# Optimization experiments

Measured on AMD Instinct MI355X. Metric: run time of the kernel, lower is better.

## Reference

```python
import jax, jax.numpy as jnp
import numpy as np

N = 20000      # nodes
E = 320000     # edges (avg in-degree 16)
R = 100        # relation types
F = 256        # in_ent_feats == out_ent_feats == in_rel_feats
H = 8          # heads
D = F // H     # head dim = 32
HOP = 5        # PPR hops
ALPHA = 0.1
SLOPE = 0.2    # LeakyReLU negative slope


def _ln(x, g, b, eps=1e-5):
    m = x.mean(-1, keepdims=True)
    v = ((x - m) ** 2).mean(-1, keepdims=True)
    return (x - m) / jnp.sqrt(v + eps) * g + b


def setup_inputs() -> dict:
    key = jax.random.key(0)
    ks = jax.random.split(key, 12)
    s = 1.0 / np.sqrt(F)
    ent_feat = jax.random.normal(ks[0], (N, F), jnp.float32)
    rel_feat = jax.random.normal(ks[1], (R, F), jnp.float32)
    W_head = jax.random.normal(ks[2], (F, F), jnp.float32) * s
    W_tail = jax.random.normal(ks[3], (F, F), jnp.float32) * s
    W_ent = jax.random.normal(ks[4], (F, F), jnp.float32) * s
    W_rel = jax.random.normal(ks[5], (F, F), jnp.float32) * s
    attn = jax.random.normal(ks[6], (1, H, D), jnp.float32) * s
    ln_ent_g = jnp.ones((F,), jnp.float32); ln_ent_b = jnp.zeros((F,), jnp.float32)
    ln_rel_g = jnp.ones((F,), jnp.float32); ln_rel_b = jnp.zeros((F,), jnp.float32)
    ln_ff_g = jnp.ones((F,), jnp.float32); ln_ff_b = jnp.zeros((F,), jnp.float32)
    W1 = jax.random.normal(ks[7], (F, 4 * F), jnp.float32) * s
    b1 = jnp.zeros((4 * F,), jnp.float32)
    W2 = jax.random.normal(ks[8], (4 * F, F), jnp.float32) * (0.5 * s)
    b2 = jnp.zeros((F,), jnp.float32)
    src = jax.random.randint(ks[9], (E,), 0, N, dtype=jnp.int32)
    # every node must have in-degree >= 1 (DGL raises on 0-in-degree nodes)
    dst = jnp.concatenate([jnp.arange(N, dtype=jnp.int32),
                           jax.random.randint(ks[10], (E - N,), 0, N, dtype=jnp.int32)])
    rid = jax.random.randint(ks[11], (E,), 0, R, dtype=jnp.int32)
    return {"ent_feat": ent_feat, "rel_feat": rel_feat,
            "W_head": W_head, "W_tail": W_tail, "W_ent": W_ent, "W_rel": W_rel,
            "attn": attn,
            "ln_ent_g": ln_ent_g, "ln_ent_b": ln_ent_b,
            "ln_rel_g": ln_rel_g, "ln_rel_b": ln_rel_b,
            "ln_ff_g": ln_ff_g, "ln_ff_b": ln_ff_b,
            "W1": W1, "b1": b1, "W2": W2, "b2": b2,
            "src": src, "dst": dst, "rid": rid}


def reference(ent_feat, rel_feat, W_head, W_tail, W_ent, W_rel, attn,
              ln_ent_g, ln_ent_b, ln_rel_g, ln_rel_b, ln_ff_g, ln_ff_b,
              W1, b1, W2, b2, src, dst, rid):
    n = ent_feat.shape[0]
    x = _ln(ent_feat, ln_ent_g, ln_ent_b)                 # [N,F]
    fh = (x @ W_head).reshape(n, H, D)                    # 'eh'
    ftl = (x @ W_tail).reshape(n, H, D)                   # 'et'
    fen = (x @ W_ent).reshape(n, H, D)                    # 'ft'
    r = _ln(rel_feat, ln_rel_g, ln_rel_b)
    fr = (r @ W_rel).reshape(-1, H, D)[rid]               # [E,H,D]
    # relational edge attention score
    e = jax.nn.leaky_relu(fh[src] * ftl[dst] * fr, SLOPE)
    e = (e * attn).sum(-1)                                # [E,H]
    # e_mul_v with log in-degree, scaled by head_dim
    deg = jax.ops.segment_sum(jnp.ones((src.shape[0],), e.dtype), dst, num_segments=n)
    e = e * (jnp.log(deg)[dst])[:, None] / D
    # edge softmax over incoming edges of each dst node, per head
    m = jax.lax.stop_gradient(jax.ops.segment_max(e, dst, num_segments=n))
    ex = jnp.exp(e - m[dst])
    denom = jax.ops.segment_sum(ex, dst, num_segments=n)
    a = ex / denom[dst]                                   # [E,H]
    # PPR-style diffusion aggregation
    feat0 = fen
    feat = fen
    for _ in range(HOP):
        msg = feat[src] * a[:, :, None]                   # [E,H,D]
        agg = jax.ops.segment_sum(msg, dst, num_segments=n)
        feat = (1.0 - ALPHA) * agg + ALPHA * feat0
    # residual (Identity since in_ent_feats == out_ent_feats)
    rst = feat + ent_feat.reshape(n, H, D)
    rst = rst.reshape(n, F)
    # position-wise feed-forward with pre-LN and residual
    y = _ln(rst, ln_ff_g, ln_ff_b)
    ff = jax.nn.relu(y @ W1 + b1) @ W2 + b2
    return ff + rst
```

## Files before the change

kernel.cpp:

```cpp
#include <hip/hip_runtime.h>

#define N_NODES 20000
#define N_EDGES 320000
#define N_REL   100
#define FDIM    256
#define NHEAD   8
#define HDIM    32
#define SCAN_BLOCKS ((N_NODES + 255) / 256)

using short8 = __attribute__((ext_vector_type(8))) short;
using f32x4  = __attribute__((ext_vector_type(4))) float;

__device__ inline unsigned short f2bf(float f) {
    union { float f; unsigned int u; } v; v.f = f;
    unsigned int r = v.u + 0x7fff + ((v.u >> 16) & 1);
    return (unsigned short)(r >> 16);
}
__device__ inline float bf2f(unsigned short u) {
    union { unsigned int i; float f; } v; v.i = ((unsigned int)u) << 16; return v.f;
}
__device__ inline float4 bf4(ushort4 u) {
    return make_float4(bf2f(u.x), bf2f(u.y), bf2f(u.z), bf2f(u.w));
}
__device__ inline void unpack8(float* d, uint4 u) {
    union { unsigned int u; float f; } t;
    t.u = u.x << 16;         d[0] = t.f;
    t.u = u.x & 0xffff0000u; d[1] = t.f;
    t.u = u.y << 16;         d[2] = t.f;
    t.u = u.y & 0xffff0000u; d[3] = t.f;
    t.u = u.z << 16;         d[4] = t.f;
    t.u = u.z & 0xffff0000u; d[5] = t.f;
    t.u = u.w << 16;         d[6] = t.f;
    t.u = u.w & 0xffff0000u; d[7] = t.f;
}
__device__ inline void fma8(float* acc, uint4 u, float w) {
    union { unsigned int u; float f; } t;
    t.u = u.x << 16;         acc[0] += w * t.f;
    t.u = u.x & 0xffff0000u; acc[1] += w * t.f;
    t.u = u.y << 16;         acc[2] += w * t.f;
    t.u = u.y & 0xffff0000u; acc[3] += w * t.f;
    t.u = u.z << 16;         acc[4] += w * t.f;
    t.u = u.z & 0xffff0000u; acc[5] += w * t.f;
    t.u = u.w << 16;         acc[6] += w * t.f;
    t.u = u.w & 0xffff0000u; acc[7] += w * t.f;
}
__device__ __forceinline__ void g2lds16(const unsigned short* g, unsigned short* l) {
    __builtin_amdgcn_global_load_lds(
        (const __attribute__((address_space(1))) unsigned int*)g,
        (__attribute__((address_space(3))) unsigned int*)l,
        16, 0, 0);
}

__device__ inline void xcd_tile(int* m0, int* n0, int tm, int tn) {
    int nwg  = gridDim.x * gridDim.y;
    int wgid = blockIdx.x + blockIdx.y * gridDim.x;
    int q = nwg >> 3, r = nwg & 7;
    int xcd = wgid & 7, pos = wgid >> 3;
    int nid = (xcd < r ? xcd * (q + 1) : r * (q + 1) + (xcd - r) * q) + pos;
    int gy = gridDim.y;
    int bx = nid / gy;
    int by = nid - bx * gy;
    *m0 = bx * tm;
    *n0 = by * tn;
}

__global__ __launch_bounds__(64) void ln_fused_kernel(
    const float* __restrict__ ent, const float* __restrict__ rel,
    const float* __restrict__ ge, const float* __restrict__ be,
    const float* __restrict__ gr, const float* __restrict__ br,
    unsigned short* __restrict__ xb, unsigned short* __restrict__ rlnb)
{
    int row = blockIdx.x;
    const float *in, *g, *b; unsigned short* out; int r;
    if (row < N_NODES) { in = ent; g = ge; b = be; out = xb;   r = row; }
    else               { in = rel; g = gr; b = br; out = rlnb; r = row - N_NODES; }
    int tid = threadIdx.x;
    const float4 v = *(const float4*)(in + (size_t)r * FDIM + tid * 4);
    float s = v.x + v.y + v.z + v.w;
    float q = v.x * v.x + v.y * v.y + v.z * v.z + v.w * v.w;
    #pragma unroll
    for (int d = 1; d < 64; d <<= 1) { s += __shfl_xor(s, d); q += __shfl_xor(q, d); }
    float mean = s * (1.0f / FDIM);
    float var  = q * (1.0f / FDIM) - mean * mean;
    float inv  = rsqrtf(var + 1e-5f);
    float4 gg = *(const float4*)(g + tid * 4);
    float4 bb = *(const float4*)(b + tid * 4);
    ushort4 o;
    o.x = f2bf((v.x - mean) * inv * gg.x + bb.x);
    o.y = f2bf((v.y - mean) * inv * gg.y + bb.y);
    o.z = f2bf((v.z - mean) * inv * gg.z + bb.z);
    o.w = f2bf((v.w - mean) * inv * gg.w + bb.w);
    *(ushort4*)(out + (size_t)r * FDIM + tid * 4) = o;
}

__global__ __launch_bounds__(64) void rst_ln_kernel(
    const unsigned short* __restrict__ feat, const float* __restrict__ ent,
    const float* __restrict__ g, const float* __restrict__ b,
    float* __restrict__ rst, unsigned short* __restrict__ y)
{
    int row = blockIdx.x;
    int tid = threadIdx.x;
    const float4 f = bf4(*(const ushort4*)(feat + (size_t)row * FDIM + tid * 4));
    const float4 e = *(const float4*)(ent + (size_t)row * FDIM + tid * 4);
    float4 r;
    r.x = f.x + e.x; r.y = f.y + e.y; r.z = f.z + e.z; r.w = f.w + e.w;
    *(float4*)(rst + (size_t)row * FDIM + tid * 4) = r;
    float s = r.x + r.y + r.z + r.w;
    float q = r.x * r.x + r.y * r.y + r.z * r.z + r.w * r.w;
    #pragma unroll
    for (int d = 1; d < 64; d <<= 1) { s += __shfl_xor(s, d); q += __shfl_xor(q, d); }
    float mean = s * (1.0f / FDIM);
    float var  = q * (1.0f / FDIM) - mean * mean;
    float inv  = rsqrtf(var + 1e-5f);
    float4 gg = *(const float4*)(g + tid * 4);
    float4 bb = *(const float4*)(b + tid * 4);
    ushort4 o;
    o.x = f2bf((r.x - mean) * inv * gg.x + bb.x);
    o.y = f2bf((r.y - mean) * inv * gg.y + bb.y);
    o.z = f2bf((r.z - mean) * inv * gg.z + bb.z);
    o.w = f2bf((r.w - mean) * inv * gg.w + bb.w);
    *(ushort4*)(y + (size_t)row * FDIM + tid * 4) = o;
}

__global__ void transpose_all_kernel(
    const float* __restrict__ Wh, const float* __restrict__ Wt_,
    const float* __restrict__ We, const float* __restrict__ Wr,
    const float* __restrict__ W1, const float* __restrict__ W2,
    unsigned short* __restrict__ WtP, unsigned short* __restrict__ WtR,
    unsigned short* __restrict__ W1t, unsigned short* __restrict__ W2t)
{
    int idx = blockIdx.x * 256 + threadIdx.x;
    if (idx < 196608) {
        int seg = idx >> 16, r = idx & 65535;
        const float* W = (seg == 0) ? Wh : (seg == 1) ? Wt_ : We;
        int n = r >> 8, k = r & 255;
        WtP[idx] = f2bf(W[k * 256 + n]);
    } else if (idx < 262144) {
        int r = idx - 196608;
        int n = r >> 8, k = r & 255;
        WtR[r] = f2bf(Wr[k * 256 + n]);
    } else if (idx < 524288) {
        int r = idx - 262144;
        int n = r >> 8, k = r & 255;
        W1t[r] = f2bf(W1[k * 1024 + n]);
    } else if (idx < 786432) {
        int r = idx - 524288;
        int n = r >> 10, k = r & 1023;
        W2t[r] = f2bf(W2[k * 256 + n]);
    }
}

__global__ __launch_bounds__(256) void mfma_gemm_bt(
    const unsigned short* __restrict__ A, const unsigned short* __restrict__ Bt,
    const float* __restrict__ bias, const float* __restrict__ add,
    float* __restrict__ Cf, unsigned short* __restrict__ Cb,
    int M, int K, int N, int relu)
{
    __shared__ unsigned short As[2][128 * 32];
    __shared__ unsigned short Bs[2][128 * 32];
    int tid  = threadIdx.x;
    int wave = tid >> 6, lane = tid & 63;
    int quad = lane >> 4, l16 = lane & 15;
    int m0, n0;
    xcd_tile(&m0, &n0, 128, 128);
    int wr = (wave >> 1) * 64, wc = (wave & 1) * 64;

    f32x4 acc[4][4] = {};

    int cA = tid, cB = tid + 256;
    int rA0 = cA >> 2, kA0 = (cA & 3) * 8;
    int rB0 = cB >> 2, kB0 = (cB & 3) * 8;
    int rA = m0 + rA0; if (rA >= M) rA = M - 1;
    int rB = m0 + rB0; if (rB >= M) rB = M - 1;
    const unsigned short* gA0 = A + (size_t)rA * K + kA0;
    const unsigned short* gA1 = A + (size_t)rB * K + kB0;
    const unsigned short* gB0 = Bt + (size_t)(n0 + rA0) * K + kA0;
    const unsigned short* gB1 = Bt + (size_t)(n0 + rB0) * K + kB0;

    g2lds16(gA0, As[0] + cA * 8);
    g2lds16(gA1, As[0] + cB * 8);
    g2lds16(gB0, Bs[0] + cA * 8);
    g2lds16(gB1, Bs[0] + cB * 8);
    __syncthreads();

    int cur = 0;
    for (int k0 = 0; k0 < K; k0 += 32) {
        int k1 = k0 + 32;
        if (k1 < K) {
            int nb = cur ^ 1;
            g2lds16(gA0 + k1, As[nb] + cA * 8);
            g2lds16(gA1 + k1, As[nb] + cB * 8);
            g2lds16(gB0 + k1, Bs[nb] + cA * 8);
            g2lds16(gB1 + k1, Bs[nb] + cB * 8);
        }
        short8 af[4], bfr[4];
        #pragma unroll
        for (int i = 0; i < 4; ++i)
            af[i] = *(const short8*)(As[cur] + (wr + i * 16 + l16) * 32 + quad * 8);
        #pragma unroll
        for (int j = 0; j < 4; ++j)
            bfr[j] = *(const short8*)(Bs[cur] + (wc + j * 16 + l16) * 32 + quad * 8);
        #pragma unroll
        for (int i = 0; i < 4; ++i)
            #pragma unroll
            for (int j = 0; j < 4; ++j)
                acc[i][j] = __builtin_amdgcn_mfma_f32_16x16x32_bf16(
                    af[i], bfr[j], acc[i][j], 0, 0, 0);
        __syncthreads();
        cur ^= 1;
    }

    #pragma unroll
    for (int i = 0; i < 4; ++i) {
        #pragma unroll
        for (int j = 0; j < 4; ++j) {
            int col = n0 + wc + j * 16 + l16;
            float bsv = bias ? bias[col] : 0.0f;
            #pragma unroll
            for (int r = 0; r < 4; ++r) {
                int row = m0 + wr + i * 16 + quad * 4 + r;
                if (row < M) {
                    float v = acc[i][j][r] + bsv;
                    if (relu) v = fmaxf(v, 0.0f);
                    if (add)  v += add[(size_t)row * N + col];
                    if (Cf) Cf[(size_t)row * N + col] = v;
                    else    Cb[(size_t)row * N + col] = f2bf(v);
                }
            }
        }
    }
}

__global__ __launch_bounds__(256) void mfma_gemm64_bt(
    const unsigned short* __restrict__ A, const unsigned short* __restrict__ Bt,
    const float* __restrict__ bias, const float* __restrict__ add,
    float* __restrict__ Cf, int M, int K, int N)
{
    __shared__ unsigned short As[2][64 * 32];
    __shared__ unsigned short Bs[2][128 * 32];
    int tid  = threadIdx.x;
    int wave = tid >> 6, lane = tid & 63;
    int quad = lane >> 4, l16 = lane & 15;
    int m0, n0;
    xcd_tile(&m0, &n0, 64, 128);
    int wc = wave * 32;

    f32x4 acc[4][2] = {};

    int rA0 = tid >> 2, kA0 = (tid & 3) * 8;
    int cB0 = tid, cB1 = tid + 256;
    int rB0 = cB0 >> 2, kB0 = (cB0 & 3) * 8;
    int rB1 = cB1 >> 2, kB1 = (cB1 & 3) * 8;
    int rA = m0 + rA0; if (rA >= M) rA = M - 1;
    const unsigned short* gA  = A + (size_t)rA * K + kA0;
    const unsigned short* gB0 = Bt + (size_t)(n0 + rB0) * K + kB0;
    const unsigned short* gB1 = Bt + (size_t)(n0 + rB1) * K + kB1;

    g2lds16(gA,  As[0] + tid * 8);
    g2lds16(gB0, Bs[0] + cB0 * 8);
    g2lds16(gB1, Bs[0] + cB1 * 8);
    __syncthreads();

    int cur = 0;
    for (int k0 = 0; k0 < K; k0 += 32) {
        int k1 = k0 + 32;
        if (k1 < K) {
            int nb = cur ^ 1;
            g2lds16(gA + k1,  As[nb] + tid * 8);
            g2lds16(gB0 + k1, Bs[nb] + cB0 * 8);
            g2lds16(gB1 + k1, Bs[nb] + cB1 * 8);
        }
        short8 af[4], bfr[2];
        #pragma unroll
        for (int i = 0; i < 4; ++i)
            af[i] = *(const short8*)(As[cur] + (i * 16 + l16) * 32 + quad * 8);
        #pragma unroll
        for (int j = 0; j < 2; ++j)
            bfr[j] = *(const short8*)(Bs[cur] + (wc + j * 16 + l16) * 32 + quad * 8);
        #pragma unroll
        for (int i = 0; i < 4; ++i)
            #pragma unroll
            for (int j = 0; j < 2; ++j)
                acc[i][j] = __builtin_amdgcn_mfma_f32_16x16x32_bf16(
                    af[i], bfr[j], acc[i][j], 0, 0, 0);
        __syncthreads();
        cur ^= 1;
    }

    #pragma unroll
    for (int i = 0; i < 4; ++i) {
        #pragma unroll
        for (int j = 0; j < 2; ++j) {
            int col = n0 + wc + j * 16 + l16;
            float bsv = bias ? bias[col] : 0.0f;
            #pragma unroll
            for (int r = 0; r < 4; ++r) {
                int row = m0 + i * 16 + quad * 4 + r;
                if (row < M) {
                    float v = acc[i][j][r] + bsv;
                    if (add) v += add[(size_t)row * N + col];
                    Cf[(size_t)row * N + col] = v;
                }
            }
        }
    }
}

__global__ void count_kernel(const int* __restrict__ dst, int* __restrict__ deg, int E)
{
    int i = blockIdx.x * blockDim.x + threadIdx.x;
    if (i < E) atomicAdd(&deg[dst[i]], 1);
}

__global__ __launch_bounds__(256) void scan1_kernel(
    const int* __restrict__ deg, int* __restrict__ offsets, int* __restrict__ bsum, int n)
{
    __shared__ int tmp[256];
    int tid = threadIdx.x;
    int i = blockIdx.x * 256 + tid;
    int v = (i < n) ? deg[i] : 0;
    tmp[tid] = v;
    __syncthreads();
    for (int d = 1; d < 256; d <<= 1) {
        int u = (tid >= d) ? tmp[tid - d] : 0;
        __syncthreads();
        tmp[tid] += u;
        __syncthreads();
    }
    if (i < n) offsets[i] = tmp[tid] - v;
    if (tid == 255) bsum[blockIdx.x] = tmp[255];
}

__global__ __launch_bounds__(128) void scan2_kernel(int* __restrict__ bsum, int nb)
{
    __shared__ int tmp[128];
    int tid = threadIdx.x;
    int v = (tid < nb) ? bsum[tid] : 0;
    tmp[tid] = v;
    __syncthreads();
    for (int d = 1; d < 128; d <<= 1) {
        int u = (tid >= d) ? tmp[tid - d] : 0;
        __syncthreads();
        tmp[tid] += u;
        __syncthreads();
    }
    if (tid < nb) bsum[tid] = tmp[tid] - v;
}

__global__ __launch_bounds__(256) void scan3_kernel(
    const int* __restrict__ deg, int* __restrict__ offsets,
    const int* __restrict__ bsum, int* __restrict__ cursor,
    float* __restrict__ logdeg, int n, int E)
{
    int i = blockIdx.x * 256 + threadIdx.x;
    if (i < n) {
        int o = offsets[i] + bsum[blockIdx.x];
        offsets[i] = o;
        cursor[i]  = o;
        logdeg[i]  = logf((float)deg[i]);
    }
    if (i == 0) offsets[n] = E;
}

__global__ void scatter_kernel(const int* __restrict__ dst, const int* __restrict__ src,
                               const int* __restrict__ rid, int* __restrict__ cursor,
                               int* __restrict__ csr_src, int* __restrict__ csr_rid, int E)
{
    int i = blockIdx.x * blockDim.x + threadIdx.x;
    if (i < E) {
        int p = atomicAdd(&cursor[dst[i]], 1);
        csr_src[p] = src[i];
        csr_rid[p] = rid[i];
    }
}

__global__ __launch_bounds__(256) void edge_score_csr_kernel(
    const unsigned short* __restrict__ proj,
    const unsigned short* __restrict__ frel,
    const float* __restrict__ attn,
    const int* __restrict__ csr_src, const int* __restrict__ csr_rid,
    const int* __restrict__ offsets, const float* __restrict__ logdeg,
    float* __restrict__ csr_a, float* __restrict__ invd, int n)
{
    int node = blockIdx.x * 4 + (threadIdx.x >> 6);
    if (node >= n) return;
    int tid = threadIdx.x & 63;
    int g = tid >> 4, li = tid & 15;
    int start = offsets[node], end = offsets[node + 1];
    float scale = logdeg[node] * (1.0f / 32.0f);

    float tv[16], at[16];
    {
        const unsigned short* tp = proj + (size_t)node * 768 + 256 + li * 16;
        uint4 a0 = *(const uint4*)tp, a1 = *(const uint4*)(tp + 8);
        unpack8(tv, a0); unpack8(tv + 8, a1);
        const float4* ap = (const float4*)(attn + li * 16);
        float4 f;
        f = ap[0]; at[0] = f.x; at[1] = f.y; at[2]  = f.z; at[3]  = f.w;
        f = ap[1]; at[4] = f.x; at[5] = f.y; at[6]  = f.z; at[7]  = f.w;
        f = ap[2]; at[8] = f.x; at[9] = f.y; at[10] = f.z; at[11] = f.w;
        f = ap[3]; at[12] = f.x; at[13] = f.y; at[14] = f.z; at[15] = f.w;
    }

    float denom = 0.f;
    for (int p = start; p < end; p += 8) {
        int  pe[2]; bool va[2]; uint4 h0[2], h1[2], r0[2], r1[2];
        #pragma unroll
        for (int t = 0; t < 2; ++t) {
            pe[t] = p + t * 4 + g;
            va[t] = pe[t] < end;
            int q = va[t] ? pe[t] : end - 1;
            int s = csr_src[q], r = csr_rid[q];
            const unsigned short* hp = proj + (size_t)s * 768 + li * 16;
            const unsigned short* rp = frel + (size_t)r * FDIM + li * 16;
            h0[t] = *(const uint4*)hp; h1[t] = *(const uint4*)(hp + 8);
            r0[t] = *(const uint4*)rp; r1[t] = *(const uint4*)(rp + 8);
        }
        #pragma unroll
        for (int t = 0; t < 2; ++t) {
            float hv[16], rv[16];
            unpack8(hv, h0[t]); unpack8(hv + 8, h1[t]);
            unpack8(rv, r0[t]); unpack8(rv + 8, r1[t]);
            float sum = 0.f;
            #pragma unroll
            for (int k = 0; k < 16; ++k) {
                float m = hv[k] * tv[k] * rv[k];
                m = (m > 0.f) ? m : 0.2f * m;
                sum += m * at[k];
            }
            sum += __shfl_xor(sum, 1);
            float ex = __expf(sum * scale);
            if (va[t] && ((li & 1) == 0)) {
                csr_a[(size_t)pe[t] * NHEAD + (li >> 1)] = ex;
                denom += ex;
            }
        }
    }
    denom += __shfl_xor(denom, 16);
    denom += __shfl_xor(denom, 32);
    if (g == 0 && (li & 1) == 0)
        invd[node * NHEAD + (li >> 1)] = 1.0f / denom;
}

__global__ __launch_bounds__(256) void diffuse_kernel(
    const unsigned short* __restrict__ fin, int fin_stride,
    const unsigned short* __restrict__ feat0,
    const float* __restrict__ a, const float* __restrict__ invd,
    const int* __restrict__ csr_src,
    const int* __restrict__ offsets, unsigned short* __restrict__ fout, int n)
{
    int node = blockIdx.x * 4 + (threadIdx.x >> 6);
    if (node >= n) return;
    int tid = threadIdx.x & 63;
    int g = tid >> 4, li = tid & 15;
    int hh = li >> 1;
    int start = offsets[node], end = offsets[node + 1];
    float wnorm = invd[node * NHEAD + hh];
    float acc[16] = {};

    for (int p = start; p < end; p += 16) {
        uint4 u0[4], u1[4]; float w[4];
        #pragma unroll
        for (int t = 0; t < 4; ++t) {
            int pe = p + t * 4 + g;
            int q = (pe < end) ? pe : end - 1;
            int s = csr_src[q];
            w[t] = (pe < end) ? a[(size_t)q * NHEAD + hh] : 0.0f;
            const unsigned short* rp = fin + (size_t)s * fin_stride + li * 16;
            u0[t] = *(const uint4*)(rp);
            u1[t] = *(const uint4*)(rp + 8);
        }
        #pragma unroll
        for (int t = 0; t < 4; ++t) {
            fma8(acc + 0, u0[t], w[t]);
            fma8(acc + 8, u1[t], w[t]);
        }
    }
    #pragma unroll
    for (int k = 0; k < 16; ++k) {
        acc[k] += __shfl_xor(acc[k], 16);
        acc[k] += __shfl_xor(acc[k], 32);
    }
    if (g == 0) {
        const unsigned short* f0p = feat0 + (size_t)node * 768 + li * 16;
        uint4 f0a = *(const uint4*)(f0p);
        uint4 f0b = *(const uint4*)(f0p + 8);
        float f0[16];
        unpack8(f0, f0a); unpack8(f0 + 8, f0b);
        unsigned short o[16];
        #pragma unroll
        for (int k = 0; k < 16; ++k)
            o[k] = f2bf(0.9f * acc[k] * wnorm + 0.1f * f0[k]);
        uint4* dst4 = (uint4*)(fout + (size_t)node * FDIM + li * 16);
        dst4[0] = *(uint4*)(o);
        dst4[1] = *(uint4*)(o + 8);
    }
}

extern "C" void kernel_launch(void* const* d_in, const int* in_sizes, int n_in,
                              void* d_out, int out_size, void* d_ws, size_t ws_size,
                              hipStream_t stream)
{
    const float* ent_feat = (const float*)d_in[0];
    const float* rel_feat = (const float*)d_in[1];
    const float* W_head   = (const float*)d_in[2];
    const float* W_tail   = (const float*)d_in[3];
    const float* W_ent    = (const float*)d_in[4];
    const float* W_rel    = (const float*)d_in[5];
    const float* attn     = (const float*)d_in[6];
    const float* ln_ent_g = (const float*)d_in[7];
    const float* ln_ent_b = (const float*)d_in[8];
    const float* ln_rel_g = (const float*)d_in[9];
    const float* ln_rel_b = (const float*)d_in[10];
    const float* ln_ff_g  = (const float*)d_in[11];
    const float* ln_ff_b  = (const float*)d_in[12];
    const float* W1       = (const float*)d_in[13];
    const float* b1       = (const float*)d_in[14];
    const float* W2       = (const float*)d_in[15];
    const float* b2       = (const float*)d_in[16];
    const int*   src      = (const int*)d_in[17];
    const int*   dst      = (const int*)d_in[18];
    const int*   rid      = (const int*)d_in[19];
    float* out = (float*)d_out;

    char* base = (char*)d_ws;
    auto carve = [&](size_t bytes) { char* p = base; base += (bytes + 255) & ~(size_t)255; return p; };
    unsigned short* xb    = (unsigned short*)carve((size_t)N_NODES * FDIM * 2);
    unsigned short* projb = (unsigned short*)carve((size_t)N_NODES * 768 * 2);
    unsigned short* rlnb  = (unsigned short*)carve((size_t)N_REL * FDIM * 2);
    unsigned short* frelb = (unsigned short*)carve((size_t)N_REL * FDIM * 2);
    unsigned short* WtP   = (unsigned short*)carve((size_t)768 * FDIM * 2);
    unsigned short* WtR   = (unsigned short*)carve((size_t)FDIM * FDIM * 2);
    unsigned short* W1t   = (unsigned short*)carve((size_t)1024 * FDIM * 2);
    unsigned short* W2t   = (unsigned short*)carve((size_t)FDIM * 1024 * 2);
    unsigned short* hb0   = (unsigned short*)carve((size_t)N_NODES * FDIM * 2);
    unsigned short* hb1   = (unsigned short*)carve((size_t)N_NODES * FDIM * 2);
    unsigned short* yb    = (unsigned short*)carve((size_t)N_NODES * FDIM * 2);
    unsigned short* t1b   = (unsigned short*)carve((size_t)N_NODES * 1024 * 2);
    float* rst     = (float*)carve((size_t)N_NODES * FDIM * 4);
    float* csr_a   = (float*)carve(((size_t)N_EDGES * NHEAD + 256) * 4);
    float* invd    = (float*)carve((size_t)N_NODES * NHEAD * 4);
    int*   csr_src = (int*)carve((size_t)(N_EDGES + 64) * 4);
    int*   csr_rid = (int*)carve((size_t)(N_EDGES + 64) * 4);
    int*   deg     = (int*)carve((size_t)N_NODES * 4);
    float* logdeg  = (float*)carve((size_t)N_NODES * 4);
    int*   offsets = (int*)carve((size_t)(N_NODES + 1) * 4);
    int*   cursor  = (int*)carve((size_t)N_NODES * 4);
    int*   bsum    = (int*)carve((size_t)SCAN_BLOCKS * 4);

    hipMemsetAsync(deg, 0, (size_t)N_NODES * 4, stream);

    ln_fused_kernel<<<N_NODES + N_REL, 64, 0, stream>>>(
        ent_feat, rel_feat, ln_ent_g, ln_ent_b, ln_rel_g, ln_rel_b, xb, rlnb);

    transpose_all_kernel<<<786432 / 256, 256, 0, stream>>>(
        W_head, W_tail, W_ent, W_rel, W1, W2, WtP, WtR, W1t, W2t);

    dim3 gproj((N_NODES + 127) / 128, 768 / 128);
    mfma_gemm_bt<<<gproj, 256, 0, stream>>>(xb, WtP, nullptr, nullptr, nullptr, projb,
                                            N_NODES, FDIM, 768, 0);
    dim3 grel(1, FDIM / 128);
    mfma_gemm_bt<<<grel, 256, 0, stream>>>(rlnb, WtR, nullptr, nullptr, nullptr, frelb,
                                           N_REL, FDIM, FDIM, 0);

    count_kernel<<<(N_EDGES + 255) / 256, 256, 0, stream>>>(dst, deg, N_EDGES);
    scan1_kernel<<<SCAN_BLOCKS, 256, 0, stream>>>(deg, offsets, bsum, N_NODES);
    scan2_kernel<<<1, 128, 0, stream>>>(bsum, SCAN_BLOCKS);
    scan3_kernel<<<SCAN_BLOCKS, 256, 0, stream>>>(deg, offsets, bsum, cursor, logdeg,
                                                  N_NODES, N_EDGES);
    scatter_kernel<<<(N_EDGES + 255) / 256, 256, 0, stream>>>(dst, src, rid, cursor,
                                                              csr_src, csr_rid, N_EDGES);

    edge_score_csr_kernel<<<(N_NODES + 3) / 4, 256, 0, stream>>>(
        projb, frelb, attn, csr_src, csr_rid, offsets, logdeg, csr_a, invd, N_NODES);

    const unsigned short* fen = projb + 512;
    int gdif = (N_NODES + 3) / 4;
    diffuse_kernel<<<gdif, 256, 0, stream>>>(fen, 768, fen, csr_a, invd, csr_src, offsets, hb0, N_NODES);
    diffuse_kernel<<<gdif, 256, 0, stream>>>(hb0, FDIM, fen, csr_a, invd, csr_src, offsets, hb1, N_NODES);
    diffuse_kernel<<<gdif, 256, 0, stream>>>(hb1, FDIM, fen, csr_a, invd, csr_src, offsets, hb0, N_NODES);
    diffuse_kernel<<<gdif, 256, 0, stream>>>(hb0, FDIM, fen, csr_a, invd, csr_src, offsets, hb1, N_NODES);
    diffuse_kernel<<<gdif, 256, 0, stream>>>(hb1, FDIM, fen, csr_a, invd, csr_src, offsets, hb0, N_NODES);

    rst_ln_kernel<<<N_NODES, 64, 0, stream>>>(hb0, ent_feat, ln_ff_g, ln_ff_b, rst, yb);

    dim3 gff1((N_NODES + 127) / 128, 1024 / 128);
    mfma_gemm_bt<<<gff1, 256, 0, stream>>>(yb, W1t, b1, nullptr, nullptr, t1b,
                                           N_NODES, FDIM, 1024, 1);
    dim3 gff2((N_NODES + 63) / 64, FDIM / 128);
    mfma_gemm64_bt<<<gff2, 256, 0, stream>>>(t1b, W2t, b2, rst, out,
                                             N_NODES, 1024, FDIM);
}
```

Measured before the change: 469.7 us.

## Load full K=256 tiles into swizzled LDS for GEMMs, hoist LDS reads in 64-row GEMM

```diff
diff --git a/kernel.cpp b/kernel.cpp
--- a/kernel.cpp
+++ b/kernel.cpp
@@ -150,14 +150,13 @@
     }
 }
 
-__global__ __launch_bounds__(256) void mfma_gemm_bt(
+__global__ __launch_bounds__(256) void mfma_gemm_k256(
     const unsigned short* __restrict__ A, const unsigned short* __restrict__ Bt,
-    const float* __restrict__ bias, const float* __restrict__ add,
-    float* __restrict__ Cf, unsigned short* __restrict__ Cb,
-    int M, int K, int N, int relu)
-{
-    __shared__ unsigned short As[2][128 * 32];
-    __shared__ unsigned short Bs[2][128 * 32];
+    const float* __restrict__ bias, unsigned short* __restrict__ Cb,
+    int M, int N, int relu)
+{
+    __shared__ unsigned short As[128 * 256];
+    __shared__ unsigned short Bs[128 * 256];
     int tid  = threadIdx.x;
     int wave = tid >> 6, lane = tid & 63;
     int quad = lane >> 4, l16 = lane & 15;
@@ -165,49 +164,43 @@
     xcd_tile(&m0, &n0, 128, 128);
     int wr = (wave >> 1) * 64, wc = (wave & 1) * 64;
 
+    int trow = tid >> 5;
+    int tcol = (tid & 31) * 16;
+    #pragma unroll
+    for (int j = 0; j < 16; ++j) {
+        int row  = j * 8 + trow;
+        int koff = tcol ^ ((row & 7) << 4);
+        int gra  = m0 + row; if (gra >= M) gra = M - 1;
+        g2lds16(A  + (size_t)gra * 256        + (koff >> 1),
+                As + row * 256 + (tcol >> 1));
+        g2lds16(Bt + (size_t)(n0 + row) * 256 + (koff >> 1),
+                Bs + row * 256 + (tcol >> 1));
+    }
+    __syncthreads();
+
     f32x4 acc[4][4] = {};
-
-    int cA = tid, cB = tid + 256;
-    int rA0 = cA >> 2, kA0 = (cA & 3) * 8;
-    int rB0 = cB >> 2, kB0 = (cB & 3) * 8;
-    int rA = m0 + rA0; if (rA >= M) rA = M - 1;
-    int rB = m0 + rB0; if (rB >= M) rB = M - 1;
-    const unsigned short* gA0 = A + (size_t)rA * K + kA0;
-    const unsigned short* gA1 = A + (size_t)rB * K + kB0;
-    const unsigned short* gB0 = Bt + (size_t)(n0 + rA0) * K + kA0;
-    const unsigned short* gB1 = Bt + (size_t)(n0 + rB0) * K + kB0;
-
-    g2lds16(gA0, As[0] + cA * 8);
-    g2lds16(gA1, As[0] + cB * 8);
-    g2lds16(gB0, Bs[0] + cA * 8);
-    g2lds16(gB1, Bs[0] + cB * 8);
-    __syncthreads();
-
-    int cur = 0;
-    for (int k0 = 0; k0 < K; k0 += 32) {
-        int k1 = k0 + 32;
-        if (k1 < K) {
-            int nb = cur ^ 1;
-            g2lds16(gA0 + k1, As[nb] + cA * 8);
-            g2lds16(gA1 + k1, As[nb] + cB * 8);
-            g2lds16(gB0 + k1, Bs[nb] + cA * 8);
-            g2lds16(gB1 + k1, Bs[nb] + cB * 8);
-        }
+    #pragma unroll
+    for (int kk = 0; kk < 8; ++kk) {
         short8 af[4], bfr[4];
-        #pragma unroll
-        for (int i = 0; i < 4; ++i)
-            af[i] = *(const short8*)(As[cur] + (wr + i * 16 + l16) * 32 + quad * 8);
-        #pragma unroll
-        for (int j = 0; j < 4; ++j)
-            bfr[j] = *(const short8*)(Bs[cur] + (wc + j * 16 + l16) * 32 + quad * 8);
+        int kb = kk * 64 + quad * 16;
+        #pragma unroll
+        for (int i = 0; i < 4; ++i) {
+            int row = wr + i * 16 + l16;
+            int off = row * 512 + (kb ^ ((row & 7) << 4));
+            af[i] = *(const short8*)((const char*)As + off);
+        }
+        #pragma unroll
+        for (int j = 0; j < 4; ++j) {
+            int row = wc + j * 16 + l16;
+            int off = row * 512 + (kb ^ ((row & 7) << 4));
+            bfr[j] = *(const short8*)((const char*)Bs + off);
+        }
         #pragma unroll
         for (int i = 0; i < 4; ++i)
             #pragma unroll
             for (int j = 0; j < 4; ++j)
                 acc[i][j] = __builtin_amdgcn_mfma_f32_16x16x32_bf16(
                     af[i], bfr[j], acc[i][j], 0, 0, 0);
-        __syncthreads();
-        cur ^= 1;
     }
 
     #pragma unroll
@@ -222,9 +215,7 @@
                 if (row < M) {
                     float v = acc[i][j][r] + bsv;
                     if (relu) v = fmaxf(v, 0.0f);
-                    if (add)  v += add[(size_t)row * N + col];
-                    if (Cf) Cf[(size_t)row * N + col] = v;
-                    else    Cb[(size_t)row * N + col] = f2bf(v);
+                    Cb[(size_t)row * N + col] = f2bf(v);
                 }
             }
         }
@@ -263,6 +254,13 @@
 
     int cur = 0;
     for (int k0 = 0; k0 < K; k0 += 32) {
+        short8 af[4], bfr[2];
+        #pragma unroll
+        for (int i = 0; i < 4; ++i)
+            af[i] = *(const short8*)(As[cur] + (i * 16 + l16) * 32 + quad * 8);
+        #pragma unroll
+        for (int j = 0; j < 2; ++j)
+            bfr[j] = *(const short8*)(Bs[cur] + (wc + j * 16 + l16) * 32 + quad * 8);
         int k1 = k0 + 32;
         if (k1 < K) {
             int nb = cur ^ 1;
@@ -270,13 +268,6 @@
             g2lds16(gB0 + k1, Bs[nb] + cB0 * 8);
             g2lds16(gB1 + k1, Bs[nb] + cB1 * 8);
         }
-        short8 af[4], bfr[2];
-        #pragma unroll
-        for (int i = 0; i < 4; ++i)
-            af[i] = *(const short8*)(As[cur] + (i * 16 + l16) * 32 + quad * 8);
-        #pragma unroll
-        for (int j = 0; j < 2; ++j)
-            bfr[j] = *(const short8*)(Bs[cur] + (wc + j * 16 + l16) * 32 + quad * 8);
         #pragma unroll
         for (int i = 0; i < 4; ++i)
             #pragma unroll
@@ -557,11 +548,11 @@
         W_head, W_tail, W_ent, W_rel, W1, W2, WtP, WtR, W1t, W2t);
 
     dim3 gproj((N_NODES + 127) / 128, 768 / 128);
-    mfma_gemm_bt<<<gproj, 256, 0, stream>>>(xb, WtP, nullptr, nullptr, nullptr, projb,
-                                            N_NODES, FDIM, 768, 0);
+    mfma_gemm_k256<<<gproj, 256, 0, stream>>>(xb, WtP, nullptr, projb,
+                                              N_NODES, 768, 0);
     dim3 grel(1, FDIM / 128);
-    mfma_gemm_bt<<<grel, 256, 0, stream>>>(rlnb, WtR, nullptr, nullptr, nullptr, frelb,
-                                           N_REL, FDIM, FDIM, 0);
+    mfma_gemm_k256<<<grel, 256, 0, stream>>>(rlnb, WtR, nullptr, frelb,
+                                             N_REL, FDIM, 0);
 
     count_kernel<<<(N_EDGES + 255) / 256, 256, 0, stream>>>(dst, deg, N_EDGES);
     scan1_kernel<<<SCAN_BLOCKS, 256, 0, stream>>>(deg, offsets, bsum, N_NODES);
@@ -585,8 +576,8 @@
     rst_ln_kernel<<<N_NODES, 64, 0, stream>>>(hb0, ent_feat, ln_ff_g, ln_ff_b, rst, yb);
 
     dim3 gff1((N_NODES + 127) / 128, 1024 / 128);
-    mfma_gemm_bt<<<gff1, 256, 0, stream>>>(yb, W1t, b1, nullptr, nullptr, t1b,
-                                           N_NODES, FDIM, 1024, 1);
+    mfma_gemm_k256<<<gff1, 256, 0, stream>>>(yb, W1t, b1, t1b,
+                                             N_NODES, 1024, 1);
     dim3 gff2((N_NODES + 63) / 64, FDIM / 128);
     mfma_gemm64_bt<<<gff2, 256, 0, stream>>>(t1b, W2t, b2, rst, out,
                                              N_NODES, 1024, FDIM);
```

After: 494.2 us. 1.05x slower.

## Fuse first diffusion hop into edge score kernel; hoist LDS fragment loads

Applied to the files above, without the earlier changes.

```diff
diff --git a/kernel.cpp b/kernel.cpp
--- a/kernel.cpp
+++ b/kernel.cpp
@@ -263,6 +263,13 @@
 
     int cur = 0;
     for (int k0 = 0; k0 < K; k0 += 32) {
+        short8 af[4], bfr[2];
+        #pragma unroll
+        for (int i = 0; i < 4; ++i)
+            af[i] = *(const short8*)(As[cur] + (i * 16 + l16) * 32 + quad * 8);
+        #pragma unroll
+        for (int j = 0; j < 2; ++j)
+            bfr[j] = *(const short8*)(Bs[cur] + (wc + j * 16 + l16) * 32 + quad * 8);
         int k1 = k0 + 32;
         if (k1 < K) {
             int nb = cur ^ 1;
@@ -270,13 +277,6 @@
             g2lds16(gB0 + k1, Bs[nb] + cB0 * 8);
             g2lds16(gB1 + k1, Bs[nb] + cB1 * 8);
         }
-        short8 af[4], bfr[2];
-        #pragma unroll
-        for (int i = 0; i < 4; ++i)
-            af[i] = *(const short8*)(As[cur] + (i * 16 + l16) * 32 + quad * 8);
-        #pragma unroll
-        for (int j = 0; j < 2; ++j)
-            bfr[j] = *(const short8*)(Bs[cur] + (wc + j * 16 + l16) * 32 + quad * 8);
         #pragma unroll
         for (int i = 0; i < 4; ++i)
             #pragma unroll
@@ -374,13 +374,14 @@
     }
 }
 
-__global__ __launch_bounds__(256) void edge_score_csr_kernel(
+__global__ __launch_bounds__(256) void score_hop1_kernel(
     const unsigned short* __restrict__ proj,
     const unsigned short* __restrict__ frel,
     const float* __restrict__ attn,
     const int* __restrict__ csr_src, const int* __restrict__ csr_rid,
     const int* __restrict__ offsets, const float* __restrict__ logdeg,
-    float* __restrict__ csr_a, float* __restrict__ invd, int n)
+    float* __restrict__ csr_a, float* __restrict__ invd,
+    unsigned short* __restrict__ fout, int n)
 {
     int node = blockIdx.x * 4 + (threadIdx.x >> 6);
     if (node >= n) return;
@@ -402,44 +403,60 @@
         f = ap[3]; at[12] = f.x; at[13] = f.y; at[14] = f.z; at[15] = f.w;
     }
 
+    float acc[16] = {};
     float denom = 0.f;
-    for (int p = start; p < end; p += 8) {
-        int  pe[2]; bool va[2]; uint4 h0[2], h1[2], r0[2], r1[2];
-        #pragma unroll
-        for (int t = 0; t < 2; ++t) {
-            pe[t] = p + t * 4 + g;
-            va[t] = pe[t] < end;
-            int q = va[t] ? pe[t] : end - 1;
-            int s = csr_src[q], r = csr_rid[q];
-            const unsigned short* hp = proj + (size_t)s * 768 + li * 16;
-            const unsigned short* rp = frel + (size_t)r * FDIM + li * 16;
-            h0[t] = *(const uint4*)hp; h1[t] = *(const uint4*)(hp + 8);
-            r0[t] = *(const uint4*)rp; r1[t] = *(const uint4*)(rp + 8);
+    for (int p = start; p < end; p += 4) {
+        int e = p + g;
+        bool va = e < end;
+        int q = va ? e : end - 1;
+        int s = csr_src[q], r = csr_rid[q];
+        const unsigned short* hp = proj + (size_t)s * 768 + li * 16;
+        const unsigned short* rp = frel + (size_t)r * FDIM + li * 16;
+        uint4 h0 = *(const uint4*)hp,        h1 = *(const uint4*)(hp + 8);
+        uint4 r0 = *(const uint4*)rp,        r1 = *(const uint4*)(rp + 8);
+        uint4 e0 = *(const uint4*)(hp + 512), e1 = *(const uint4*)(hp + 520);
+        float hv[16], rv[16];
+        unpack8(hv, h0); unpack8(hv + 8, h1);
+        unpack8(rv, r0); unpack8(rv + 8, r1);
+        float sum = 0.f;
+        #pragma unroll
+        for (int k = 0; k < 16; ++k) {
+            float m = hv[k] * tv[k] * rv[k];
+            m = (m > 0.f) ? m : 0.2f * m;
+            sum += m * at[k];
         }
-        #pragma unroll
-        for (int t = 0; t < 2; ++t) {
-            float hv[16], rv[16];
-            unpack8(hv, h0[t]); unpack8(hv + 8, h1[t]);
-            unpack8(rv, r0[t]); unpack8(rv + 8, r1[t]);
-            float sum = 0.f;
-            #pragma unroll
-            for (int k = 0; k < 16; ++k) {
-                float m = hv[k] * tv[k] * rv[k];
-                m = (m > 0.f) ? m : 0.2f * m;
-                sum += m * at[k];
-            }
-            sum += __shfl_xor(sum, 1);
-            float ex = __expf(sum * scale);
-            if (va[t] && ((li & 1) == 0)) {
-                csr_a[(size_t)pe[t] * NHEAD + (li >> 1)] = ex;
-                denom += ex;
-            }
-        }
+        sum += __shfl_xor(sum, 1);
+        float ex = va ? __expf(sum * scale) : 0.f;
+        if (va && ((li & 1) == 0))
+            csr_a[(size_t)e * NHEAD + (li >> 1)] = ex;
+        denom += ex;
+        fma8(acc + 0, e0, ex);
+        fma8(acc + 8, e1, ex);
     }
     denom += __shfl_xor(denom, 16);
     denom += __shfl_xor(denom, 32);
+    #pragma unroll
+    for (int k = 0; k < 16; ++k) {
+        acc[k] += __shfl_xor(acc[k], 16);
+        acc[k] += __shfl_xor(acc[k], 32);
+    }
+    float wn = 1.0f / denom;
     if (g == 0 && (li & 1) == 0)
-        invd[node * NHEAD + (li >> 1)] = 1.0f / denom;
+        invd[node * NHEAD + (li >> 1)] = wn;
+    if (g == 0) {
+        const unsigned short* f0p = proj + (size_t)node * 768 + 512 + li * 16;
+        uint4 f0a = *(const uint4*)(f0p);
+        uint4 f0b = *(const uint4*)(f0p + 8);
+        float f0[16];
+        unpack8(f0, f0a); unpack8(f0 + 8, f0b);
+        unsigned short o[16];
+        #pragma unroll
+        for (int k = 0; k < 16; ++k)
+            o[k] = f2bf(0.9f * acc[k] * wn + 0.1f * f0[k]);
+        uint4* dst4 = (uint4*)(fout + (size_t)node * FDIM + li * 16);
+        dst4[0] = *(uint4*)(o);
+        dst4[1] = *(uint4*)(o + 8);
+    }
 }
 
 __global__ __launch_bounds__(256) void diffuse_kernel(
@@ -571,12 +588,12 @@
     scatter_kernel<<<(N_EDGES + 255) / 256, 256, 0, stream>>>(dst, src, rid, cursor,
                                                               csr_src, csr_rid, N_EDGES);
 
-    edge_score_csr_kernel<<<(N_NODES + 3) / 4, 256, 0, stream>>>(
-        projb, frelb, attn, csr_src, csr_rid, offsets, logdeg, csr_a, invd, N_NODES);
+    score_hop1_kernel<<<(N_NODES + 3) / 4, 256, 0, stream>>>(
+        projb, frelb, attn, csr_src, csr_rid, offsets, logdeg,
+        csr_a, invd, hb0, N_NODES);
 
     const unsigned short* fen = projb + 512;
     int gdif = (N_NODES + 3) / 4;
-    diffuse_kernel<<<gdif, 256, 0, stream>>>(fen, 768, fen, csr_a, invd, csr_src, offsets, hb0, N_NODES);
     diffuse_kernel<<<gdif, 256, 0, stream>>>(hb0, FDIM, fen, csr_a, invd, csr_src, offsets, hb1, N_NODES);
     diffuse_kernel<<<gdif, 256, 0, stream>>>(hb1, FDIM, fen, csr_a, invd, csr_src, offsets, hb0, N_NODES);
     diffuse_kernel<<<gdif, 256, 0, stream>>>(hb0, FDIM, fen, csr_a, invd, csr_src, offsets, hb1, N_NODES);
```

New measurement: 460.1 us. 2.0% less time.
